# Kernel tuning notes

Hardware: AMD Instinct MI355X
Metric: run time of the kernel (lower is better)

The kernel has to match this reference:

```python
import jax, jax.numpy as jnp
import numpy as np

NUM_HEADS = 16
HEAD_DIM = 128
EMBED = NUM_HEADS * HEAD_DIM  # 2048
BATCH, SEQ = 2, 2048


def setup_inputs() -> dict:
    key = jax.random.key(0)
    k1, k2 = jax.random.split(key)
    x = jax.random.normal(k1, (BATCH, SEQ, EMBED), dtype=jnp.float32)
    W = jax.random.normal(k2, (EMBED, 3 * EMBED), dtype=jnp.float32) * 0.02
    b = jnp.zeros((3 * EMBED,), dtype=jnp.float32)
    return {"x": x, "W": W, "b": b}


def _rotate_half(u):
    u1, u2 = jnp.split(u, 2, axis=-1)
    return jnp.concatenate([-u2, u1], axis=-1)


def reference(x, W, b):
    B, S, E = x.shape
    H, D = NUM_HEADS, HEAD_DIM
    # Fused QKV projection: [B,S,E] @ [E,3E] -> [B,S,3E]
    qkv = jnp.einsum('bse,ef->bsf', x, W) + b
    qkv = qkv.reshape(B, S, 3, H, D)
    q, k, v = qkv[:, :, 0], qkv[:, :, 1], qkv[:, :, 2]  # each [B,S,H,D]
    # Module's rotary embedding: sin/cos over arange(S*D), shared across heads
    t = jnp.arange(S * D, dtype=jnp.float32).reshape(1, S, 1, D)
    sin, cos = jnp.sin(t), jnp.cos(t)
    q = q * cos + _rotate_half(q) * sin
    k = k * cos + _rotate_half(k) * sin
    # Scaled dot-product attention over sequence, per head
    scale = 1.0 / jnp.sqrt(jnp.float32(D))
    attn = jnp.einsum('bqhd,bkhd->bhqk', q, k) * scale  # [B,H,S,S]
    w = jax.nn.softmax(attn, axis=-1)
    out = jnp.einsum('bhqk,bkhd->bqhd', w, v)  # [B,S,H,D]
    return out
```

## Files before the change

### kernel.cpp

```cpp
#include <hip/hip_runtime.h>
#include <stdint.h>

typedef unsigned short u16;
typedef __attribute__((ext_vector_type(8))) short bf16x8;
typedef __attribute__((ext_vector_type(4))) float f32x4;

#define NUM_B 2
#define SEQ   2048
#define SEQP  2080
#define NH    16
#define HD    128
#define EMB   2048
#define N3    6144
#define MM    4096
#define QT    64
#define WQ    32
#define KT    32
#define NTILE (SEQ / KT)

#define BM 128
#define BN 256
#define BK 64
#define NT_K (EMB / BK)

__device__ __forceinline__ u16 f2bf(float f) {
  union { float f; unsigned u; } c; c.f = f;
  return (u16)((c.u + 0x7FFFu + ((c.u >> 16) & 1u)) >> 16);
}
__device__ __forceinline__ void async16(const void* g, void* l) {
  __builtin_amdgcn_global_load_lds(
      (const __attribute__((address_space(1))) void*)g,
      (__attribute__((address_space(3))) void*)l, 16, 0, 0);
}

#define GBAR()   asm volatile("s_barrier" ::: "memory")
#define WLGKM0() asm volatile("s_waitcnt lgkmcnt(0)" ::: "memory")


__global__ void k_cvt_bf16(const float* __restrict__ in, u16* __restrict__ out, int n4) {
  int i = blockIdx.x * blockDim.x + threadIdx.x;
  if (i >= n4) return;
  const float4 v = ((const float4*)in)[i];
  ushort4 o;
  o.x = f2bf(v.x); o.y = f2bf(v.y); o.z = f2bf(v.z); o.w = f2bf(v.w);
  ((ushort4*)out)[i] = o;
}

__global__ void k_transpose_w(const float* __restrict__ W, u16* __restrict__ Wt) {
  __shared__ float t[32][33];
  int n0 = blockIdx.x * 32, k0 = blockIdx.y * 32;
  int tx = threadIdx.x, ty = threadIdx.y;
  #pragma unroll
  for (int i = ty; i < 32; i += 8)
    t[i][tx] = W[(size_t)(k0 + i) * N3 + n0 + tx];
  __syncthreads();
  #pragma unroll
  for (int i = ty; i < 32; i += 8)
    Wt[(size_t)(n0 + i) * EMB + k0 + tx] = f2bf(t[tx][i]);
}

__global__ void k_sincos(float2* __restrict__ tab) {
  int i = blockIdx.x * blockDim.x + threadIdx.x;
  double t = (double)i;
  tab[i] = make_float2((float)cos(t), (float)sin(t));
}

__global__ __launch_bounds__(512, 2) void k_gemm_qkv(
    const u16* __restrict__ xb, const u16* __restrict__ wt,
    const float* __restrict__ bias, const float2* __restrict__ tab,
    u16* __restrict__ qb, u16* __restrict__ kb, u16* __restrict__ vbt)
{
  __shared__ __align__(16) u16 lsA[2][BM * BK];
  __shared__ __align__(16) u16 lsB[2][BN * BK];
  const int tid = threadIdx.x;
  const int wave = tid >> 6, lane = tid & 63;
  const int lq = lane & 15, lr = lane >> 4;
  const int wr = wave >> 2, wc = wave & 3;
  const int m0 = blockIdx.y * BM, n0 = blockIdx.x * BN;

  auto stageA = [&](int t, int buf) {
    const int kt = t * BK;
    #pragma unroll
    for (int ii = 0; ii < 2; ++ii) {
      int s = ii * 512 + tid;
      int row = s >> 3, gq = (s & 7) ^ (row & 7);
      async16(xb + (size_t)(m0 + row) * EMB + kt + gq * 8, &lsA[buf][s * 8]);
    }
  };
  auto stageB = [&](int t, int buf, int half) {
    const int kt = t * BK;
    #pragma unroll
    for (int ii = 0; ii < 2; ++ii) {
      int s = ii * 512 + tid;
      int row = s >> 3, gq = (s & 7) ^ (row & 7);
      async16(wt + (size_t)(n0 + half * 128 + row) * EMB + kt + gq * 8,
              &lsB[buf][half * 8192 + s * 8]);
    }
  };

  f32x4 acc[4][4];
  #pragma unroll
  for (int i = 0; i < 4; ++i)
    #pragma unroll
    for (int j = 0; j < 4; ++j)
      acc[i][j] = f32x4{0.f, 0.f, 0.f, 0.f};

  int rbase[4];
  #pragma unroll
  for (int nf = 0; nf < 4; ++nf)
    rbase[nf] = ((wc >> 1) * 128 + (nf >> 1) * 64 + (wc & 1) * 32 + (nf & 1) * 16 + lq) * BK;
  const int aRow0 = (wr * 64 + lq) * BK;
  int qsw[2];
  qsw[0] = ((0 + lr) ^ (lq & 7)) * 8;
  qsw[1] = ((4 + lr) ^ (lq & 7)) * 8;

  stageA(0, 0); stageB(0, 0, 0); stageB(0, 0, 1);
  stageB(1, 1, 0); stageB(1, 1, 1);
  asm volatile("s_waitcnt vmcnt(4)" ::: "memory");
  GBAR();

  for (int t = 0; t < NT_K; ++t) {
    const int p = t & 1;
    const u16* Ap = lsA[p];
    const u16* Bp = lsB[p];
    bf16x8 bfr[4][2];

    #pragma unroll
    for (int q = 0; q < 2; ++q) {
      bf16x8 afr[2][2];
      if (q == 0) {
        #pragma unroll
        for (int nf = 0; nf < 4; ++nf)
          #pragma unroll
          for (int kk = 0; kk < 2; ++kk)
            bfr[nf][kk] = *(const bf16x8*)(Bp + rbase[nf] + qsw[kk]);
      }
      #pragma unroll
      for (int mfl = 0; mfl < 2; ++mfl)
        #pragma unroll
        for (int kk = 0; kk < 2; ++kk)
          afr[mfl][kk] = *(const bf16x8*)(Ap + aRow0 + (q * 32 + mfl * 16) * BK + qsw[kk]);

      if (q == 0) {
        if (t + 1 < NT_K) stageA(t + 1, 1 - p);
      } else {
        if (t + 2 < NT_K) {
          stageB(t + 2, p, 0);
          stageB(t + 2, p, 1);
          asm volatile("s_waitcnt vmcnt(4)" ::: "memory");
        } else if (t + 1 < NT_K) {
          asm volatile("s_waitcnt vmcnt(0)" ::: "memory");
        }
      }
      GBAR();
      WLGKM0();
      __builtin_amdgcn_s_setprio(1);
      #pragma unroll
      for (int kk = 0; kk < 2; ++kk)
        #pragma unroll
        for (int mfl = 0; mfl < 2; ++mfl)
          #pragma unroll
          for (int nf = 0; nf < 4; ++nf)
            acc[q * 2 + mfl][nf] = __builtin_amdgcn_mfma_f32_16x16x32_bf16(
                afr[mfl][kk], bfr[nf][kk], acc[q * 2 + mfl][nf], 0, 0, 0);
      __builtin_amdgcn_s_setprio(0);
      GBAR();
    }
  }

  const int w = n0 >> 11;
  const int h = ((n0 & 2047) >> 7) + (wc >> 1);
  float bb[4];
  int dloc[4];
  #pragma unroll
  for (int nf = 0; nf < 4; ++nf) {
    dloc[nf] = (nf >> 1) * 64 + (wc & 1) * 32 + (nf & 1) * 16 + lq;
    bb[nf] = bias[n0 + (wc >> 1) * 128 + dloc[nf]];
  }

  if (w == 2) {
    #pragma unroll
    for (int mfg = 0; mfg < 4; ++mfg) {
      int mg0 = m0 + wr * 64 + mfg * 16 + lr * 4;
      int b = mg0 >> 11, s0 = mg0 & 2047;
      #pragma unroll
      for (int nf = 0; nf < 4; ++nf) {
        int d = dloc[nf];
        ushort4 pk;
        pk.x = f2bf(acc[mfg][nf][0] + bb[nf]);
        pk.y = f2bf(acc[mfg][nf][1] + bb[nf]);
        pk.z = f2bf(acc[mfg][nf][2] + bb[nf]);
        pk.w = f2bf(acc[mfg][nf][3] + bb[nf]);
        *(ushort4*)(vbt + ((size_t)(b * NH + h) * HD + d) * SEQP + s0) = pk;
      }
    }
  } else {
    u16* basep = (w == 0) ? qb : kb;
    const float qs = (w == 0) ? 0.12751569843736827f : 1.0f;
    #pragma unroll
    for (int mfg = 0; mfg < 4; ++mfg)
      #pragma unroll
      for (int r = 0; r < 4; ++r) {
        int mg = m0 + wr * 64 + mfg * 16 + lr * 4 + r;
        int b = mg >> 11, s = mg & 2047;
        u16* dst = basep + ((size_t)(b * NH + h) * SEQ + s) * HD;
        #pragma unroll
        for (int nf = 0; nf < 2; ++nf) {
          int d1 = dloc[nf];
          float c1 = acc[mfg][nf][r]     + bb[nf];
          float c2 = acc[mfg][nf + 2][r] + bb[nf + 2];
          float2 s1 = tab[s * HD + d1];
          float2 s2 = tab[s * HD + d1 + 64];
          dst[d1]      = f2bf((c1 * s1.x - c2 * s1.y) * qs);
          dst[d1 + 64] = f2bf((c2 * s2.x + c1 * s2.y) * qs);
        }
      }
  }
}

__global__ __launch_bounds__(128, 2) void k_flash(
    const u16* __restrict__ qb, const u16* __restrict__ kb,
    const u16* __restrict__ vbt, float* __restrict__ out)
{
  __shared__ __align__(16) u16 lsK[2][KT * HD];
  __shared__ __align__(16) u16 lsV[2][HD * KT];
  __shared__ __align__(16) u16 lsP[2][WQ * KT];

  const int tid = threadIdx.x;
  const int wave = tid >> 6, lane = tid & 63;
  const int lq = lane & 15, lr = lane >> 4;
  const int i = blockIdx.x;
  const int xcd = i & 7, j = i >> 3;
  const int bh = xcd * 4 + (j >> 5);
  const int q0 = (j & 31) * QT;
  const u16* Qg = qb + ((size_t)bh * SEQ + q0 + wave * WQ) * HD;
  const u16* Kg = kb + (size_t)bh * SEQ * HD;
  const u16* Vg = vbt + (size_t)bh * HD * SEQP;

  auto stage = [&](int tile, int buf) {
    const int k0 = tile * KT;
    #pragma unroll
    for (int ii = 0; ii < 4; ++ii) {
      int c = tid + ii * 128;
      int key = c >> 4, grp = c & 15;
      async16(Kg + (size_t)(k0 + key) * HD + ((grp ^ (key & 7)) * 8), lsK[buf] + c * 8);
    }
    #pragma unroll
    for (int ii = 0; ii < 4; ++ii) {
      int c = tid + ii * 128;
      int d = c >> 2, g2 = c & 3;
      async16(Vg + (size_t)d * SEQP + k0 + ((g2 ^ ((d >> 1) & 3)) * 8), lsV[buf] + c * 8);
    }
  };

  stage(0, 0);

  bf16x8 qf[2][4];
  #pragma unroll
  for (int qq = 0; qq < 2; ++qq)
    #pragma unroll
    for (int ks = 0; ks < 4; ++ks)
      qf[qq][ks] = *(const bf16x8*)(Qg + (size_t)(qq * 16 + lq) * HD + ks * 32 + lr * 8);

  f32x4 acc_o[2][8];
  float lsum[2] = {0.f, 0.f};
  #pragma unroll
  for (int mb = 0; mb < 2; ++mb)
    #pragma unroll
    for (int nb = 0; nb < 8; ++nb) acc_o[mb][nb] = f32x4{0.f, 0.f, 0.f, 0.f};

  for (int t = 0; t < NTILE; ++t) {
    const int p = t & 1;
    __syncthreads();
    if (t + 1 < NTILE) stage(t + 1, 1 - p);

    f32x4 sacc[2][2];
    #pragma unroll
    for (int kbi = 0; kbi < 2; ++kbi)
      #pragma unroll
      for (int qq = 0; qq < 2; ++qq) sacc[kbi][qq] = f32x4{0.f, 0.f, 0.f, 0.f};
    #pragma unroll
    for (int ks = 0; ks < 4; ++ks) {
      bf16x8 kf[2];
      #pragma unroll
      for (int kbi = 0; kbi < 2; ++kbi) {
        int key = kbi * 16 + lq;
        int g = (ks * 4 + lr) ^ (key & 7);
        kf[kbi] = *(const bf16x8*)(lsK[p] + key * HD + g * 8);
      }
      #pragma unroll
      for (int kbi = 0; kbi < 2; ++kbi)
        #pragma unroll
        for (int qq = 0; qq < 2; ++qq)
          sacc[kbi][qq] = __builtin_amdgcn_mfma_f32_16x16x32_bf16(kf[kbi], qf[qq][ks], sacc[kbi][qq], 0, 0, 0);
    }

    #pragma unroll
    for (int kbi = 0; kbi < 2; ++kbi)
      #pragma unroll
      for (int qq = 0; qq < 2; ++qq) {
        float p0 = __builtin_amdgcn_exp2f(sacc[kbi][qq][0]);
        float p1 = __builtin_amdgcn_exp2f(sacc[kbi][qq][1]);
        float p2 = __builtin_amdgcn_exp2f(sacc[kbi][qq][2]);
        float p3 = __builtin_amdgcn_exp2f(sacc[kbi][qq][3]);
        lsum[qq] += (p0 + p1) + (p2 + p3);
        int row = qq * 16 + lq;
        int g = kbi * 4 + lr;
        int gp = g ^ (row & 6);
        uint2 pk;
        pk.x = (uint32_t)f2bf(p0) | ((uint32_t)f2bf(p1) << 16);
        pk.y = (uint32_t)f2bf(p2) | ((uint32_t)f2bf(p3) << 16);
        *(uint2*)(lsP[wave] + row * KT + gp * 4) = pk;
      }

    bf16x8 ap[2];
    #pragma unroll
    for (int mb = 0; mb < 2; ++mb) {
      int row = mb * 16 + lq;
      int gp = (2 * lr) ^ (row & 6);
      ap[mb] = *(const bf16x8*)(lsP[wave] + row * KT + gp * 4);
    }
    #pragma unroll
    for (int nb = 0; nb < 8; ++nb) {
      int d = nb * 16 + lq;
      int g2 = lr ^ ((d >> 1) & 3);
      bf16x8 bv = *(const bf16x8*)(lsV[p] + d * KT + g2 * 8);
      #pragma unroll
      for (int mb = 0; mb < 2; ++mb)
        acc_o[mb][nb] = __builtin_amdgcn_mfma_f32_16x16x32_bf16(ap[mb], bv[0] == bv[0] ? bv : bv, acc_o[mb][nb], 0, 0, 0);
    }
  }

  float inv[2];
  #pragma unroll
  for (int qq = 0; qq < 2; ++qq) {
    float s = lsum[qq];
    s += __shfl_xor(s, 16);
    s += __shfl_xor(s, 32);
    inv[qq] = 1.0f / s;
  }
  const int b = bh >> 4, h = bh & 15;
  #pragma unroll
  for (int mb = 0; mb < 2; ++mb)
    #pragma unroll
    for (int r = 0; r < 4; ++r) {
      float iv = __shfl(inv[mb], lr * 4 + r);
      int row = wave * WQ + mb * 16 + lr * 4 + r;
      int sq = q0 + row;
      float* op = out + (((size_t)b * SEQ + sq) * NH + h) * HD;
      #pragma unroll
      for (int nb = 0; nb < 8; ++nb)
        op[nb * 16 + lq] = acc_o[mb][nb][r] * iv;
    }
}


extern "C" void kernel_launch(void* const* d_in, const int* in_sizes, int n_in,
                              void* d_out, int out_size, void* d_ws, size_t ws_size,
                              hipStream_t stream) {
  (void)in_sizes; (void)n_in; (void)out_size; (void)ws_size;
  const float* x    = (const float*)d_in[0];
  const float* W    = (const float*)d_in[1];
  const float* bias = (const float*)d_in[2];
  float* out = (float*)d_out;

  char* p = (char*)d_ws;
  u16* xb  = (u16*)p;  p += (size_t)MM * EMB * 2;
  u16* wt  = (u16*)p;  p += (size_t)N3 * EMB * 2;
  u16* qb  = (u16*)p;  p += (size_t)NUM_B * NH * SEQ * HD * 2;
  u16* kb  = (u16*)p;  p += (size_t)NUM_B * NH * SEQ * HD * 2;
  u16* vbt = (u16*)p;  p += (size_t)NUM_B * NH * HD * SEQP * 2;
  float2* tab = (float2*)p;

  k_cvt_bf16<<<(MM * EMB / 4 + 255) / 256, 256, 0, stream>>>(x, xb, MM * EMB / 4);
  k_transpose_w<<<dim3(N3 / 32, EMB / 32), dim3(32, 8), 0, stream>>>(W, wt);
  k_sincos<<<(SEQ * HD) / 256, 256, 0, stream>>>(tab);
  k_gemm_qkv<<<dim3(N3 / BN, MM / BM), 512, 0, stream>>>(xb, wt, bias, tab, qb, kb, vbt);
  k_flash<<<SEQ / QT * NUM_B * NH, 128, 0, stream>>>(qb, kb, vbt, out);
}
```

Baseline: 260.2 us.

## Double QKV GEMM M-tile to 256 with restructured async staging pipeline

Raises the QKV projection GEMM block tile from 128x256 to 256x256, so each wave accumulates 8x4 MFMA fragments and every B tile loaded into LDS is reused across twice as many rows. The K loop is unrolled by two with A and B tile loads staged in halves across the four compute sub-steps, and the column mapping of the B fragments is permuted, with the epilogue index math updated to match. This cuts global and LDS traffic per FLOP, but doubles LDS use and accumulator registers, which may lower occupancy relative to the two-blocks-per-CU launch bound and halves the number of blocks in the grid.

```diff
diff --git a/kernel.cpp b/kernel.cpp
--- a/kernel.cpp
+++ b/kernel.cpp
@@ -18,7 +18,7 @@
 #define KT    32
 #define NTILE (SEQ / KT)
 
-#define BM 128
+#define BM 256
 #define BN 256
 #define BK 64
 #define NT_K (EMB / BK)
@@ -78,29 +78,30 @@
   const int wr = wave >> 2, wc = wave & 3;
   const int m0 = blockIdx.y * BM, n0 = blockIdx.x * BN;
 
-  auto stageA = [&](int t, int buf) {
+  auto stA = [&](int t, int half) {
     const int kt = t * BK;
     #pragma unroll
     for (int ii = 0; ii < 2; ++ii) {
       int s = ii * 512 + tid;
       int row = s >> 3, gq = (s & 7) ^ (row & 7);
-      async16(xb + (size_t)(m0 + row) * EMB + kt + gq * 8, &lsA[buf][s * 8]);
+      async16(xb + (size_t)(m0 + half * 128 + row) * EMB + kt + gq * 8,
+              &lsA[t & 1][half * 8192 + s * 8]);
     }
   };
-  auto stageB = [&](int t, int buf, int half) {
+  auto stB = [&](int t, int half) {
     const int kt = t * BK;
     #pragma unroll
     for (int ii = 0; ii < 2; ++ii) {
       int s = ii * 512 + tid;
       int row = s >> 3, gq = (s & 7) ^ (row & 7);
       async16(wt + (size_t)(n0 + half * 128 + row) * EMB + kt + gq * 8,
-              &lsB[buf][half * 8192 + s * 8]);
+              &lsB[t & 1][half * 8192 + s * 8]);
     }
   };
 
-  f32x4 acc[4][4];
-  #pragma unroll
-  for (int i = 0; i < 4; ++i)
+  f32x4 acc[8][4];
+  #pragma unroll
+  for (int i = 0; i < 8; ++i)
     #pragma unroll
     for (int j = 0; j < 4; ++j)
       acc[i][j] = f32x4{0.f, 0.f, 0.f, 0.f};
@@ -108,63 +109,81 @@
   int rbase[4];
   #pragma unroll
   for (int nf = 0; nf < 4; ++nf)
-    rbase[nf] = ((wc >> 1) * 128 + (nf >> 1) * 64 + (wc & 1) * 32 + (nf & 1) * 16 + lq) * BK;
-  const int aRow0 = (wr * 64 + lq) * BK;
+    rbase[nf] = ((wc >> 1) * 128 + (2 * (wc & 1) + (nf >> 1)) * 16 + (nf & 1) * 64 + lq) * BK;
+  const int aRow0 = (wr * 128 + lq) * BK;
   int qsw[2];
   qsw[0] = ((0 + lr) ^ (lq & 7)) * 8;
   qsw[1] = ((4 + lr) ^ (lq & 7)) * 8;
 
-  stageA(0, 0); stageB(0, 0, 0); stageB(0, 0, 1);
-  stageB(1, 1, 0); stageB(1, 1, 1);
+  stA(0, 0); stA(0, 1); stB(0, 0); stB(0, 1); stB(1, 0); stB(1, 1);
   asm volatile("s_waitcnt vmcnt(4)" ::: "memory");
   GBAR();
 
-  for (int t = 0; t < NT_K; ++t) {
-    const int p = t & 1;
-    const u16* Ap = lsA[p];
-    const u16* Bp = lsB[p];
-    bf16x8 bfr[4][2];
-
-    #pragma unroll
-    for (int q = 0; q < 2; ++q) {
-      bf16x8 afr[2][2];
-      if (q == 0) {
-        #pragma unroll
-        for (int nf = 0; nf < 4; ++nf)
+  for (int ti = 0; ti < NT_K / 2; ++ti) {
+    const int t0 = 2 * ti, t1 = t0 + 1;
+    const bool notlast = (ti < NT_K / 2 - 1);
+
+    #pragma unroll
+    for (int hp = 0; hp < 2; ++hp) {
+      const u16* Ap = lsA[hp];
+      const u16* Bp = lsB[hp];
+      bf16x8 bfr[4][2];
+
+      #pragma unroll
+      for (int q = 0; q < 4; ++q) {
+        if (q == 0) {
           #pragma unroll
-          for (int kk = 0; kk < 2; ++kk)
-            bfr[nf][kk] = *(const bf16x8*)(Bp + rbase[nf] + qsw[kk]);
-      }
-      #pragma unroll
-      for (int mfl = 0; mfl < 2; ++mfl)
-        #pragma unroll
-        for (int kk = 0; kk < 2; ++kk)
-          afr[mfl][kk] = *(const bf16x8*)(Ap + aRow0 + (q * 32 + mfl * 16) * BK + qsw[kk]);
-
-      if (q == 0) {
-        if (t + 1 < NT_K) stageA(t + 1, 1 - p);
-      } else {
-        if (t + 2 < NT_K) {
-          stageB(t + 2, p, 0);
-          stageB(t + 2, p, 1);
-          asm volatile("s_waitcnt vmcnt(4)" ::: "memory");
-        } else if (t + 1 < NT_K) {
-          asm volatile("s_waitcnt vmcnt(0)" ::: "memory");
+          for (int nf = 0; nf < 4; ++nf)
+            #pragma unroll
+            for (int kk = 0; kk < 2; ++kk)
+              bfr[nf][kk] = *(const bf16x8*)(Bp + rbase[nf] + qsw[kk]);
         }
-      }
-      GBAR();
-      WLGKM0();
-      __builtin_amdgcn_s_setprio(1);
-      #pragma unroll
-      for (int kk = 0; kk < 2; ++kk)
+        bf16x8 af[2][2];
         #pragma unroll
         for (int mfl = 0; mfl < 2; ++mfl)
           #pragma unroll
-          for (int nf = 0; nf < 4; ++nf)
-            acc[q * 2 + mfl][nf] = __builtin_amdgcn_mfma_f32_16x16x32_bf16(
-                afr[mfl][kk], bfr[nf][kk], acc[q * 2 + mfl][nf], 0, 0, 0);
-      __builtin_amdgcn_s_setprio(0);
-      GBAR();
+          for (int kk = 0; kk < 2; ++kk)
+            af[mfl][kk] = *(const bf16x8*)(Ap + aRow0 + (q * 32 + mfl * 16) * BK + qsw[kk]);
+
+        if (hp == 0) {
+          if      (q == 0) stA(t1, 0);
+          else if (q == 1) stA(t1, 1);
+          else if (q == 2) { if (notlast) stB(t0 + 2, 0); }
+          else {
+            if (notlast) {
+              stB(t0 + 2, 1);
+              asm volatile("s_waitcnt vmcnt(4)" ::: "memory");
+            } else {
+              asm volatile("s_waitcnt vmcnt(0)" ::: "memory");
+            }
+          }
+        } else {
+          if      (q == 0) { if (notlast) stA(t0 + 2, 0); }
+          else if (q == 1) { if (notlast) stA(t0 + 2, 1); }
+          else if (q == 2) { if (notlast) stB(t1 + 2, 0); }
+          else {
+            if (notlast) {
+              stB(t1 + 2, 1);
+              asm volatile("s_waitcnt vmcnt(4)" ::: "memory");
+            }
+          }
+        }
+        if (q == 0) asm volatile("s_waitcnt lgkmcnt(8)" ::: "memory");
+
+        GBAR();
+        WLGKM0();
+        __builtin_amdgcn_s_setprio(1);
+        #pragma unroll
+        for (int kk = 0; kk < 2; ++kk)
+          #pragma unroll
+          for (int mfl = 0; mfl < 2; ++mfl)
+            #pragma unroll
+            for (int nf = 0; nf < 4; ++nf)
+              acc[q * 2 + mfl][nf] = __builtin_amdgcn_mfma_f32_16x16x32_bf16(
+                  af[mfl][kk], bfr[nf][kk], acc[q * 2 + mfl][nf], 0, 0, 0);
+        __builtin_amdgcn_s_setprio(0);
+        GBAR();
+      }
     }
   }
 
@@ -174,23 +193,23 @@
   int dloc[4];
   #pragma unroll
   for (int nf = 0; nf < 4; ++nf) {
-    dloc[nf] = (nf >> 1) * 64 + (wc & 1) * 32 + (nf & 1) * 16 + lq;
+    dloc[nf] = (2 * (wc & 1) + (nf >> 1)) * 16 + (nf & 1) * 64 + lq;
     bb[nf] = bias[n0 + (wc >> 1) * 128 + dloc[nf]];
   }
 
   if (w == 2) {
     #pragma unroll
-    for (int mfg = 0; mfg < 4; ++mfg) {
-      int mg0 = m0 + wr * 64 + mfg * 16 + lr * 4;
+    for (int mf = 0; mf < 8; ++mf) {
+      int mg0 = m0 + wr * 128 + mf * 16 + lr * 4;
       int b = mg0 >> 11, s0 = mg0 & 2047;
       #pragma unroll
       for (int nf = 0; nf < 4; ++nf) {
         int d = dloc[nf];
         ushort4 pk;
-        pk.x = f2bf(acc[mfg][nf][0] + bb[nf]);
-        pk.y = f2bf(acc[mfg][nf][1] + bb[nf]);
-        pk.z = f2bf(acc[mfg][nf][2] + bb[nf]);
-        pk.w = f2bf(acc[mfg][nf][3] + bb[nf]);
+        pk.x = f2bf(acc[mf][nf][0] + bb[nf]);
+        pk.y = f2bf(acc[mf][nf][1] + bb[nf]);
+        pk.z = f2bf(acc[mf][nf][2] + bb[nf]);
+        pk.w = f2bf(acc[mf][nf][3] + bb[nf]);
         *(ushort4*)(vbt + ((size_t)(b * NH + h) * HD + d) * SEQP + s0) = pk;
       }
     }
@@ -198,17 +217,17 @@
     u16* basep = (w == 0) ? qb : kb;
     const float qs = (w == 0) ? 0.12751569843736827f : 1.0f;
     #pragma unroll
-    for (int mfg = 0; mfg < 4; ++mfg)
+    for (int mf = 0; mf < 8; ++mf)
       #pragma unroll
       for (int r = 0; r < 4; ++r) {
-        int mg = m0 + wr * 64 + mfg * 16 + lr * 4 + r;
+        int mg = m0 + wr * 128 + mf * 16 + lr * 4 + r;
         int b = mg >> 11, s = mg & 2047;
         u16* dst = basep + ((size_t)(b * NH + h) * SEQ + s) * HD;
         #pragma unroll
-        for (int nf = 0; nf < 2; ++nf) {
-          int d1 = dloc[nf];
-          float c1 = acc[mfg][nf][r]     + bb[nf];
-          float c2 = acc[mfg][nf + 2][r] + bb[nf + 2];
+        for (int pl = 0; pl < 2; ++pl) {
+          int d1 = (2 * (wc & 1) + pl) * 16 + lq;
+          float c1 = acc[mf][2 * pl][r]     + bb[2 * pl];
+          float c2 = acc[mf][2 * pl + 1][r] + bb[2 * pl + 1];
           float2 s1 = tab[s * HD + d1];
           float2 s2 = tab[s * HD + d1 + 64];
           dst[d1]      = f2bf((c1 * s1.x - c2 * s1.y) * qs);
```

Measured after the change: 245.8 us. -5.5%, faster.
